# Optimization experiments

Measured on AMD Instinct MI355X. Metric: run time of the kernel, lower is better.

The kernel has to match this reference:

```python
import jax, jax.numpy as jnp
import numpy as np

B, S, E, H = 32, 2048, 1024, 1024


def setup_inputs() -> dict:
    key = jax.random.key(0)
    k0, k1, k2, k3, k4, k5, k6 = jax.random.split(key, 7)
    hidden = jax.random.normal(k0, (B, 1, H), jnp.float32)
    encoder_outputs = jax.random.normal(k1, (B, S, E), jnp.float32)
    mask = jax.random.randint(k2, (B, S), 0, 2).astype(bool)
    mask = mask.at[:, 0].set(False)  # guarantee >=1 unmasked position per row
    sM = 1.0 / np.sqrt(E + H)
    M_w = jax.random.uniform(k3, (H, E + H), jnp.float32, -sM, sM)
    M_b = jax.random.uniform(k4, (H,), jnp.float32, -sM, sM)
    sV = 1.0 / np.sqrt(H)
    V_w = jax.random.uniform(k5, (1, H), jnp.float32, -sV, sV)
    V_b = jax.random.uniform(k6, (1,), jnp.float32, -sV, sV)
    return {"hidden": hidden, "encoder_outputs": encoder_outputs, "mask": mask,
            "M_w": M_w, "M_b": M_b, "V_w": V_w, "V_b": V_b}


def reference(hidden, encoder_outputs, mask, M_w, M_b, V_w, V_b):
    # concat([enc, H]) @ M_w.T == enc @ M_w[:, :E].T + hidden @ M_w[:, E:].T
    # (avoids materializing the B x S x (E+H) concat)
    m = (jnp.einsum('bse,he->bsh', encoder_outputs, M_w[:, :E])
         + jnp.einsum('boh,hd->boh'.replace('d', 'g'), hidden, M_w[:, E:].T)
         + M_b)
    scores = jnp.einsum('bsh,h->bs', jnp.tanh(m), V_w[0]) + V_b[0]  # B x S
    NEG = jnp.float32(-1e30)
    scores = jnp.where(mask, NEG, scores)
    weights = jax.nn.softmax(scores, axis=1)  # B x S
    weighted = jnp.einsum('bs,bse->be', weights, encoder_outputs)[:, None, :]
    return weighted, weights[:, None, :]
```

## Files before the change

### kernel.cpp

```cpp
#include <hip/hip_runtime.h>

typedef __attribute__((ext_vector_type(8))) short short8;
typedef __attribute__((ext_vector_type(4))) float floatx4;


__device__ __forceinline__ unsigned short f2bf(float f) {
    unsigned u = __float_as_uint(f);
    return (unsigned short)((u + 0x7FFFu + ((u >> 16) & 1u)) >> 16);
}
__device__ __forceinline__ unsigned pack2(float a, float b) {
    return (unsigned)f2bf(a) | ((unsigned)f2bf(b) << 16);
}

__global__ __launch_bounds__(256) void csum_kernel(const float* __restrict__ Mw,
                                                   float* __restrict__ csum) {
    int j = blockIdx.x;
    int h = (j & 3) * 256 + threadIdx.x;
    int g0 = (j >> 2) * 128;
    float p = 0.f;
    #pragma unroll 8
    for (int g = g0; g < g0 + 128; ++g) p += Mw[(size_t)g * 2048 + 1024 + h];
    atomicAdd(&csum[h], p);
}

__global__ __launch_bounds__(256) void hbias_kernel(const float* __restrict__ hidden,
                                                    const float* __restrict__ csum,
                                                    const float* __restrict__ Mb,
                                                    float* __restrict__ hbias) {
    int b = blockIdx.x;
    #pragma unroll
    for (int i = 0; i < 4; ++i) {
        int h = i * 256 + threadIdx.x;
        hbias[b * 1024 + h] = hidden[b * 1024 + h] * csum[h] + Mb[h];
    }
}

__global__ __launch_bounds__(256) void gemm_scores(const float* __restrict__ A,
                                                   const float* __restrict__ Mw,
                                                   const float* __restrict__ hbias,
                                                   const float* __restrict__ Vw,
                                                   float* __restrict__ scores) {
    __shared__ unsigned short As[2][128][32];
    __shared__ unsigned short Bs[2][128][32];

    int bid = blockIdx.x;
    int wg = (bid & 7) * (gridDim.x >> 3) + (bid >> 3);
    int mtile = wg >> 3;
    int ntile = wg & 7;

    int t = threadIdx.x;
    int r = t >> 1, cg = (t & 1) * 16;
    const float* Ap = A  + (size_t)(mtile * 128 + r) * 1024 + cg;
    const float* Bp = Mw + (size_t)(ntile * 128 + r) * 2048 + cg;

    float4 a0, a1, a2, a3, b0, b1, b2, b3;
#define LOADT(KT) { const float* ap = Ap + (KT) * 32;                              \
        a0 = *(const float4*)ap;        a1 = *(const float4*)(ap + 4);             \
        a2 = *(const float4*)(ap + 8);  a3 = *(const float4*)(ap + 12);            \
        const float* bp = Bp + (KT) * 32;                                          \
        b0 = *(const float4*)bp;        b1 = *(const float4*)(bp + 4);             \
        b2 = *(const float4*)(bp + 8);  b3 = *(const float4*)(bp + 12); }
#define WRITET(BUF) { uint4 w;                                                     \
        w.x = pack2(a0.x,a0.y); w.y = pack2(a0.z,a0.w);                            \
        w.z = pack2(a1.x,a1.y); w.w = pack2(a1.z,a1.w);                            \
        *(uint4*)&As[BUF][r][cg] = w;                                              \
        w.x = pack2(a2.x,a2.y); w.y = pack2(a2.z,a2.w);                            \
        w.z = pack2(a3.x,a3.y); w.w = pack2(a3.z,a3.w);                            \
        *(uint4*)&As[BUF][r][cg + 8] = w;                                          \
        w.x = pack2(b0.x,b0.y); w.y = pack2(b0.z,b0.w);                            \
        w.z = pack2(b1.x,b1.y); w.w = pack2(b1.z,b1.w);                            \
        *(uint4*)&Bs[BUF][r][cg] = w;                                              \
        w.x = pack2(b2.x,b2.y); w.y = pack2(b2.z,b2.w);                            \
        w.z = pack2(b3.x,b3.y); w.w = pack2(b3.z,b3.w);                            \
        *(uint4*)&Bs[BUF][r][cg + 8] = w; }

    int lane = t & 63, wave = t >> 6;
    int wr = wave >> 1, wc = wave & 1;
    int l15 = lane & 15, l4 = lane >> 4;

    floatx4 zero = {0.f, 0.f, 0.f, 0.f};
    floatx4 acc[4][4];
    #pragma unroll
    for (int m = 0; m < 4; ++m)
        #pragma unroll
        for (int n = 0; n < 4; ++n) acc[m][n] = zero;

    LOADT(0);
    WRITET(0);

    #pragma unroll 2
    for (int kt = 0; kt < 32; ++kt) {
        int cur = kt & 1;
        __syncthreads();
        if (kt < 31) LOADT(kt + 1);
        short8 af[4], bf[4];
        #pragma unroll
        for (int m = 0; m < 4; ++m)
            af[m] = *(const short8*)&As[cur][wr * 64 + m * 16 + l15][l4 * 8];
        #pragma unroll
        for (int n = 0; n < 4; ++n)
            bf[n] = *(const short8*)&Bs[cur][wc * 64 + n * 16 + l15][l4 * 8];
        #pragma unroll
        for (int m = 0; m < 4; ++m)
            #pragma unroll
            for (int n = 0; n < 4; ++n)
                acc[m][n] = __builtin_amdgcn_mfma_f32_16x16x32_bf16(af[m], bf[n], acc[m][n], 0, 0, 0);
        if (kt < 31) WRITET(cur ^ 1);
    }

    int b = mtile >> 4;
    int rowbase = mtile * 128 + wr * 64;
    int colbase = ntile * 128 + wc * 64;
    float vw[4], hb[4];
    #pragma unroll
    for (int n = 0; n < 4; ++n) {
        int h = colbase + n * 16 + l15;
        vw[n] = Vw[h];
        hb[n] = hbias[b * 1024 + h];
    }
    #pragma unroll
    for (int m = 0; m < 4; ++m) {
        #pragma unroll
        for (int j = 0; j < 4; ++j) {
            float s = 0.f;
            #pragma unroll
            for (int n = 0; n < 4; ++n)
                s += tanhf(acc[m][n][j] + hb[n]) * vw[n];
            s += __shfl_xor(s, 1); s += __shfl_xor(s, 2);
            s += __shfl_xor(s, 4); s += __shfl_xor(s, 8);
            if (l15 == 0)
                atomicAdd(&scores[rowbase + m * 16 + l4 * 4 + j], s);
        }
    }
#undef LOADT
#undef WRITET
}

__global__ __launch_bounds__(256) void softmax_kernel(const float* __restrict__ scores,
                                                      const int* __restrict__ mask,
                                                      const float* __restrict__ Vb,
                                                      float* __restrict__ wout) {
    int b = blockIdx.x, t = threadIdx.x;
    float vb = Vb[0];
    float v[8];
    float mx = -3.4e38f;
    #pragma unroll
    for (int i = 0; i < 8; ++i) {
        int s = i * 256 + t;
        float sc = scores[b * 2048 + s] + vb;
        sc = mask[b * 2048 + s] ? -1e30f : sc;
        v[i] = sc;
        mx = fmaxf(mx, sc);
    }
    #pragma unroll
    for (int off = 32; off; off >>= 1) mx = fmaxf(mx, __shfl_xor(mx, off));
    __shared__ float sm[4], ss[4];
    int wv = t >> 6, ln = t & 63;
    if (!ln) sm[wv] = mx;
    __syncthreads();
    mx = fmaxf(fmaxf(sm[0], sm[1]), fmaxf(sm[2], sm[3]));
    float sum = 0.f;
    #pragma unroll
    for (int i = 0; i < 8; ++i) { v[i] = __expf(v[i] - mx); sum += v[i]; }
    #pragma unroll
    for (int off = 32; off; off >>= 1) sum += __shfl_xor(sum, off);
    if (!ln) ss[wv] = sum;
    __syncthreads();
    sum = ss[0] + ss[1] + ss[2] + ss[3];
    float inv = 1.0f / sum;
    #pragma unroll
    for (int i = 0; i < 8; ++i) wout[b * 2048 + i * 256 + t] = v[i] * inv;
}

__global__ __launch_bounds__(256) void weighted_kernel(const float* __restrict__ enc,
                                                       const float* __restrict__ w,
                                                       float* __restrict__ out) {
    int blk = blockIdx.x;
    int b = blk >> 5;
    int ec = (blk >> 3) & 3;
    int ssg = blk & 7;
    int e = ec * 256 + threadIdx.x;
    const float* encb = enc + ((size_t)b * 2048 + ssg * 256) * 1024 + e;
    const float* wb = w + b * 2048 + ssg * 256;
    float acc = 0.f;
    #pragma unroll 8
    for (int s = 0; s < 256; ++s) acc += wb[s] * encb[(size_t)s * 1024];
    atomicAdd(&out[b * 1024 + e], acc);
}

extern "C" void kernel_launch(void* const* d_in, const int* in_sizes, int n_in,
                              void* d_out, int out_size, void* d_ws, size_t ws_size,
                              hipStream_t stream) {
    (void)in_sizes; (void)n_in; (void)ws_size;
    const float* hidden = (const float*)d_in[0];
    const float* enc    = (const float*)d_in[1];
    const int*   mask   = (const int*)d_in[2];
    const float* Mw     = (const float*)d_in[3];
    const float* Mb     = (const float*)d_in[4];
    const float* Vw     = (const float*)d_in[5];
    const float* Vb     = (const float*)d_in[6];

    float* out    = (float*)d_out;
    float* scores = (float*)d_ws;
    float* csum   = scores + 65536;
    float* hbias  = csum + 1024;

    hipMemsetAsync(d_out, 0, (size_t)out_size * sizeof(float), stream);
    hipMemsetAsync(d_ws, 0, (65536 + 1024) * sizeof(float), stream);

    hipLaunchKernelGGL(csum_kernel,    dim3(32),   dim3(256), 0, stream, Mw, csum);
    hipLaunchKernelGGL(hbias_kernel,   dim3(32),   dim3(256), 0, stream, hidden, csum, Mb, hbias);
    hipLaunchKernelGGL(gemm_scores,    dim3(4096), dim3(256), 0, stream, enc, Mw, hbias, Vw, scores);
    hipLaunchKernelGGL(softmax_kernel, dim3(32),   dim3(256), 0, stream, scores, mask, Vb, out + 32768);
    hipLaunchKernelGGL(weighted_kernel,dim3(1024), dim3(256), 0, stream, enc, out + 32768, out);
}
```

Before: 823.1 us.

## Pre-convert encoder and weights to bf16 and use direct-to-LDS GEMM loads

Adds conversion kernels that write the encoder outputs and the encoder half of M_w as bf16 into the workspace. A new GEMM then streams these through global_load_lds with a 64-wide K tile, and a new weighted-sum kernel reads the bf16 encoder copy. Together these aim to halve the bytes read in the two main passes and remove the in-loop float-to-bf16 packing. The cost is an extra full pass over the encoder (read fp32, write bf16), a large workspace requirement, bf16 rounding in the weighted sum, and an exp-based tanh approximation.

```diff
diff --git a/kernel.cpp b/kernel.cpp
--- a/kernel.cpp
+++ b/kernel.cpp
@@ -10,6 +10,42 @@
 }
 __device__ __forceinline__ unsigned pack2(float a, float b) {
     return (unsigned)f2bf(a) | ((unsigned)f2bf(b) << 16);
+}
+__device__ __forceinline__ float bf2f(unsigned short v) {
+    return __uint_as_float(((unsigned)v) << 16);
+}
+__device__ __forceinline__ float fast_tanh(float x) {
+    float e = __expf(2.f * x);
+    return 1.f - 2.f / (e + 1.f);
+}
+__device__ __forceinline__ void gll16(const void* g, void* l) {
+    __builtin_amdgcn_global_load_lds(
+        (const __attribute__((address_space(1))) unsigned int*)g,
+        (__attribute__((address_space(3))) unsigned int*)l, 16, 0, 0);
+}
+
+__global__ __launch_bounds__(256) void conv_enc(const float* __restrict__ in,
+                                                unsigned short* __restrict__ ob) {
+    size_t idx = (size_t)blockIdx.x * 256 + threadIdx.x;
+    const size_t stride = (size_t)gridDim.x * 256;
+    const size_t n8 = 67108864 / 8;
+    for (size_t i = idx; i < n8; i += stride) {
+        float4 f0 = ((const float4*)in)[2 * i];
+        float4 f1 = ((const float4*)in)[2 * i + 1];
+        uint4 w;
+        w.x = pack2(f0.x, f0.y); w.y = pack2(f0.z, f0.w);
+        w.z = pack2(f1.x, f1.y); w.w = pack2(f1.z, f1.w);
+        ((uint4*)ob)[i] = w;
+    }
+}
+
+__global__ __launch_bounds__(256) void conv_mw(const float* __restrict__ Mw,
+                                               unsigned short* __restrict__ ob) {
+    int r = blockIdx.x;
+    int c = threadIdx.x * 4;
+    float4 f = *(const float4*)&Mw[(size_t)r * 2048 + c];
+    uint2 w; w.x = pack2(f.x, f.y); w.y = pack2(f.z, f.w);
+    *(uint2*)&ob[r * 1024 + c] = w;
 }
 
 __global__ __launch_bounds__(256) void csum_kernel(const float* __restrict__ Mw,
@@ -35,6 +71,91 @@
     }
 }
 
+__global__ __launch_bounds__(256, 3) void gemm_scores2(const unsigned short* __restrict__ Ab,
+                                                       const unsigned short* __restrict__ Bb,
+                                                       const float* __restrict__ hbias,
+                                                       const float* __restrict__ Vw,
+                                                       float* __restrict__ scores) {
+    __shared__ unsigned short As[128][64];
+    __shared__ unsigned short Bs[128][64];
+
+    int bid = blockIdx.x;
+    int wg = (bid & 7) * (gridDim.x >> 3) + (bid >> 3);
+    int mtile = wg >> 3;
+    int ntile = wg & 7;
+
+    int t = threadIdx.x, lane = t & 63, wave = t >> 6;
+    int wr = wave >> 1, wc = wave & 1;
+    int l15 = lane & 15, l4 = lane >> 4;
+
+    const unsigned short* Abase = Ab + (size_t)(mtile * 128) * 1024;
+    const unsigned short* Bbase = Bb + (size_t)(ntile * 128) * 1024;
+
+    int e0 = wave * 512 + lane * 8;
+
+    floatx4 zero = {0.f, 0.f, 0.f, 0.f};
+    floatx4 acc[4][4];
+    #pragma unroll
+    for (int m = 0; m < 4; ++m)
+        #pragma unroll
+        for (int n = 0; n < 4; ++n) acc[m][n] = zero;
+
+    for (int kt = 0; kt < 16; ++kt) {
+        int k0 = kt * 64;
+        #pragma unroll
+        for (int i = 0; i < 4; ++i) {
+            int elem = i * 2048 + e0;
+            int row = elem >> 6, kk = elem & 63;
+            gll16(Abase + (size_t)row * 1024 + k0 + kk, &As[row][kk]);
+            gll16(Bbase + (size_t)row * 1024 + k0 + kk, &Bs[row][kk]);
+        }
+        __syncthreads();
+        short8 af[2][4], bf[2][4];
+        #pragma unroll
+        for (int ks = 0; ks < 2; ++ks) {
+            #pragma unroll
+            for (int m = 0; m < 4; ++m)
+                af[ks][m] = *(const short8*)&As[wr * 64 + m * 16 + l15][ks * 32 + l4 * 8];
+            #pragma unroll
+            for (int n = 0; n < 4; ++n)
+                bf[ks][n] = *(const short8*)&Bs[wc * 64 + n * 16 + l15][ks * 32 + l4 * 8];
+        }
+        #pragma unroll
+        for (int ks = 0; ks < 2; ++ks)
+            #pragma unroll
+            for (int m = 0; m < 4; ++m)
+                #pragma unroll
+                for (int n = 0; n < 4; ++n)
+                    acc[m][n] = __builtin_amdgcn_mfma_f32_16x16x32_bf16(af[ks][m], bf[ks][n], acc[m][n], 0, 0, 0);
+        __syncthreads();
+    }
+
+    int b = mtile >> 4;
+    int rowbase = mtile * 128 + wr * 64;
+    int colbase = ntile * 128 + wc * 64;
+    float vw[4], hb[4];
+    #pragma unroll
+    for (int n = 0; n < 4; ++n) {
+        int h = colbase + n * 16 + l15;
+        vw[n] = Vw[h];
+        hb[n] = hbias[b * 1024 + h];
+    }
+    #pragma unroll
+    for (int m = 0; m < 4; ++m) {
+        #pragma unroll
+        for (int j = 0; j < 4; ++j) {
+            float s = 0.f;
+            #pragma unroll
+            for (int n = 0; n < 4; ++n)
+                s += fast_tanh(acc[m][n][j] + hb[n]) * vw[n];
+            s += __shfl_xor(s, 1); s += __shfl_xor(s, 2);
+            s += __shfl_xor(s, 4); s += __shfl_xor(s, 8);
+            if (l15 == 0)
+                atomicAdd(&scores[rowbase + m * 16 + l4 * 4 + j], s);
+        }
+    }
+}
+
 __global__ __launch_bounds__(256) void gemm_scores(const float* __restrict__ A,
                                                    const float* __restrict__ Mw,
                                                    const float* __restrict__ hbias,
@@ -42,17 +163,13 @@
                                                    float* __restrict__ scores) {
     __shared__ unsigned short As[2][128][32];
     __shared__ unsigned short Bs[2][128][32];
-
     int bid = blockIdx.x;
     int wg = (bid & 7) * (gridDim.x >> 3) + (bid >> 3);
-    int mtile = wg >> 3;
-    int ntile = wg & 7;
-
+    int mtile = wg >> 3, ntile = wg & 7;
     int t = threadIdx.x;
     int r = t >> 1, cg = (t & 1) * 16;
     const float* Ap = A  + (size_t)(mtile * 128 + r) * 1024 + cg;
     const float* Bp = Mw + (size_t)(ntile * 128 + r) * 2048 + cg;
-
     float4 a0, a1, a2, a3, b0, b1, b2, b3;
 #define LOADT(KT) { const float* ap = Ap + (KT) * 32;                              \
         a0 = *(const float4*)ap;        a1 = *(const float4*)(ap + 4);             \
@@ -73,21 +190,16 @@
         w.x = pack2(b2.x,b2.y); w.y = pack2(b2.z,b2.w);                            \
         w.z = pack2(b3.x,b3.y); w.w = pack2(b3.z,b3.w);                            \
         *(uint4*)&Bs[BUF][r][cg + 8] = w; }
-
     int lane = t & 63, wave = t >> 6;
     int wr = wave >> 1, wc = wave & 1;
     int l15 = lane & 15, l4 = lane >> 4;
-
     floatx4 zero = {0.f, 0.f, 0.f, 0.f};
     floatx4 acc[4][4];
     #pragma unroll
     for (int m = 0; m < 4; ++m)
         #pragma unroll
         for (int n = 0; n < 4; ++n) acc[m][n] = zero;
-
-    LOADT(0);
-    WRITET(0);
-
+    LOADT(0); WRITET(0);
     #pragma unroll 2
     for (int kt = 0; kt < 32; ++kt) {
         int cur = kt & 1;
@@ -107,7 +219,6 @@
                 acc[m][n] = __builtin_amdgcn_mfma_f32_16x16x32_bf16(af[m], bf[n], acc[m][n], 0, 0, 0);
         if (kt < 31) WRITET(cur ^ 1);
     }
-
     int b = mtile >> 4;
     int rowbase = mtile * 128 + wr * 64;
     int colbase = ntile * 128 + wc * 64;
@@ -125,7 +236,7 @@
             float s = 0.f;
             #pragma unroll
             for (int n = 0; n < 4; ++n)
-                s += tanhf(acc[m][n][j] + hb[n]) * vw[n];
+                s += fast_tanh(acc[m][n][j] + hb[n]) * vw[n];
             s += __shfl_xor(s, 1); s += __shfl_xor(s, 2);
             s += __shfl_xor(s, 4); s += __shfl_xor(s, 8);
             if (l15 == 0)
@@ -170,6 +281,30 @@
     float inv = 1.0f / sum;
     #pragma unroll
     for (int i = 0; i < 8; ++i) wout[b * 2048 + i * 256 + t] = v[i] * inv;
+}
+
+__global__ __launch_bounds__(256) void weighted2(const unsigned short* __restrict__ encb,
+                                                 const float* __restrict__ w,
+                                                 float* __restrict__ out) {
+    int blk = blockIdx.x;
+    int b = blk >> 4, sseg = blk & 15;
+    int t = threadIdx.x;
+    int e0 = (t & 127) * 8;
+    int sr = t >> 7;
+    const unsigned short* base = encb + ((size_t)b * 2048 + sseg * 128 + sr) * 1024 + e0;
+    const float* wb = w + b * 2048 + sseg * 128 + sr;
+    float acc[8] = {0, 0, 0, 0, 0, 0, 0, 0};
+    #pragma unroll 4
+    for (int s = 0; s < 128; s += 2) {
+        float ws = wb[s];
+        short8 v = *(const short8*)(base + (size_t)s * 1024);
+        #pragma unroll
+        for (int j = 0; j < 8; ++j)
+            acc[j] += ws * bf2f((unsigned short)v[j]);
+    }
+    #pragma unroll
+    for (int j = 0; j < 8; ++j)
+        atomicAdd(&out[b * 1024 + e0 + j], acc[j]);
 }
 
 __global__ __launch_bounds__(256) void weighted_kernel(const float* __restrict__ enc,
@@ -191,7 +326,7 @@
 extern "C" void kernel_launch(void* const* d_in, const int* in_sizes, int n_in,
                               void* d_out, int out_size, void* d_ws, size_t ws_size,
                               hipStream_t stream) {
-    (void)in_sizes; (void)n_in; (void)ws_size;
+    (void)in_sizes; (void)n_in; (void)out_size;
     const float* hidden = (const float*)d_in[0];
     const float* enc    = (const float*)d_in[1];
     const int*   mask   = (const int*)d_in[2];
@@ -199,18 +334,39 @@
     const float* Mb     = (const float*)d_in[4];
     const float* Vw     = (const float*)d_in[5];
     const float* Vb     = (const float*)d_in[6];
-
-    float* out    = (float*)d_out;
-    float* scores = (float*)d_ws;
-    float* csum   = scores + 65536;
-    float* hbias  = csum + 1024;
-
-    hipMemsetAsync(d_out, 0, (size_t)out_size * sizeof(float), stream);
-    hipMemsetAsync(d_ws, 0, (65536 + 1024) * sizeof(float), stream);
-
-    hipLaunchKernelGGL(csum_kernel,    dim3(32),   dim3(256), 0, stream, Mw, csum);
-    hipLaunchKernelGGL(hbias_kernel,   dim3(32),   dim3(256), 0, stream, hidden, csum, Mb, hbias);
-    hipLaunchKernelGGL(gemm_scores,    dim3(4096), dim3(256), 0, stream, enc, Mw, hbias, Vw, scores);
-    hipLaunchKernelGGL(softmax_kernel, dim3(32),   dim3(256), 0, stream, scores, mask, Vb, out + 32768);
-    hipLaunchKernelGGL(weighted_kernel,dim3(1024), dim3(256), 0, stream, enc, out + 32768, out);
-}
+    float* out = (float*)d_out;
+
+    const size_t ENC_N = 67108864;
+    const size_t MW_N  = 1048576;
+    const size_t need  = ENC_N * 2 + MW_N * 2 + (65536 + 1024 + 32768) * 4;
+
+    if (ws_size >= need) {
+        unsigned short* encb = (unsigned short*)d_ws;
+        unsigned short* Mwb  = encb + ENC_N;
+        float* scores = (float*)(Mwb + MW_N);
+        float* csum   = scores + 65536;
+        float* hbias  = csum + 1024;
+
+        hipMemsetAsync(out, 0, 32768 * sizeof(float), stream);
+        hipMemsetAsync(scores, 0, (65536 + 1024) * sizeof(float), stream);
+
+        hipLaunchKernelGGL(conv_enc,       dim3(2048), dim3(256), 0, stream, enc, encb);
+        hipLaunchKernelGGL(conv_mw,        dim3(1024), dim3(256), 0, stream, Mw, Mwb);
+        hipLaunchKernelGGL(csum_kernel,    dim3(32),   dim3(256), 0, stream, Mw, csum);
+        hipLaunchKernelGGL(hbias_kernel,   dim3(32),   dim3(256), 0, stream, hidden, csum, Mb, hbias);
+        hipLaunchKernelGGL(gemm_scores2,   dim3(4096), dim3(256), 0, stream, encb, Mwb, hbias, Vw, scores);
+        hipLaunchKernelGGL(softmax_kernel, dim3(32),   dim3(256), 0, stream, scores, mask, Vb, out + 32768);
+        hipLaunchKernelGGL(weighted2,      dim3(512),  dim3(256), 0, stream, encb, out + 32768, out);
+    } else {
+        float* scores = (float*)d_ws;
+        float* csum   = scores + 65536;
+        float* hbias  = csum + 1024;
+        hipMemsetAsync(out, 0, 32768 * sizeof(float), stream);
+        hipMemsetAsync(scores, 0, (65536 + 1024) * sizeof(float), stream);
+        hipLaunchKernelGGL(csum_kernel,    dim3(32),   dim3(256), 0, stream, Mw, csum);
+        hipLaunchKernelGGL(hbias_kernel,   dim3(32),   dim3(256), 0, stream, hidden, csum, Mb, hbias);
+        hipLaunchKernelGGL(gemm_scores,    dim3(4096), dim3(256), 0, stream, enc, Mw, hbias, Vw, scores);
+        hipLaunchKernelGGL(softmax_kernel, dim3(32),   dim3(256), 0, stream, scores, mask, Vb, out + 32768);
+        hipLaunchKernelGGL(weighted_kernel,dim3(1024), dim3(256), 0, stream, enc, out + 32768, out);
+    }
+}
```

Result: faster. 688.9 us (-16.3%).
